# Kernel optimization log

Measured on AMD Instinct MI355X. Metric: run time of the kernel, lower is better.

Reference implementation:

```python
import jax, jax.numpy as jnp
import numpy as np

TEMP = 1.75   # temp_schedule(epoch=5, warmup=10): 2.5 - 1.5*0.5
ALPHA = 0.5   # blend_schedule(epoch=5): 0.2 + 0.6*0.5
EPS = 1e-5
HEADS = 2


def _ln(x, g, b):
    mu = x.mean(-1, keepdims=True)
    var = ((x - mu) ** 2).mean(-1, keepdims=True)
    return (x - mu) * jax.lax.rsqrt(var + EPS) * g + b


def _gelu(x):
    return jax.nn.gelu(x, approximate=False)  # torch nn.GELU default = exact erf


def _attn_pool(x, ln_g, ln_b, in_w, in_b, out_w, out_b):
    # x: [N, T, E]; nn.MultiheadAttention self-attention then mean over T
    N, T, E = x.shape
    Dh = E // HEADS
    xn = _ln(x, ln_g, ln_b)
    qkv = xn @ in_w + in_b                      # [N, T, 3E] (in_w stored [E, 3E])
    q, k, v = jnp.split(qkv, 3, axis=-1)
    q = q.reshape(N, T, HEADS, Dh).transpose(0, 2, 1, 3)
    k = k.reshape(N, T, HEADS, Dh).transpose(0, 2, 1, 3)
    v = v.reshape(N, T, HEADS, Dh).transpose(0, 2, 1, 3)
    scores = jnp.einsum('nhqd,nhkd->nhqk', q, k) / jnp.sqrt(jnp.float32(Dh))
    a = jax.nn.softmax(scores, axis=-1)
    o = jnp.einsum('nhqk,nhkd->nhqd', a, v).transpose(0, 2, 1, 3).reshape(N, T, E)
    o = o @ out_w + out_b                       # [N, T, E]
    return o.mean(axis=1)                       # [N, E]


def setup_inputs() -> dict:
    key = jax.random.key(0)
    ks = iter(jax.random.split(key, 40))
    B, L, T, D = 4, 24, 400, 1024
    H = D // 2  # 512
    G = 4       # groups
    s = 0.02
    r = lambda shp: jax.random.normal(next(ks), shp, dtype=jnp.float32) * s
    inp = {
        'x': jax.random.normal(next(ks), (B, L, T, D), dtype=jnp.float32),
        'mlp_alpha': jnp.ones((L,), jnp.float32),
        # shared MLP: LN -> Linear(D,H) -> GELU -> Linear(H,H)
        's_ln_g': jnp.ones((D,), jnp.float32), 's_ln_b': jnp.zeros((D,), jnp.float32),
        's_w1': r((D, H)), 's_b1': jnp.zeros((H,), jnp.float32),
        's_w2': r((H, H)), 's_b2': jnp.zeros((H,), jnp.float32),
        # 4 group MLPs (stacked)
        'g_ln_g': jnp.ones((G, D), jnp.float32), 'g_ln_b': jnp.zeros((G, D), jnp.float32),
        'g_w1': r((G, D, H)), 'g_b1': jnp.zeros((G, H), jnp.float32),
        'g_w2': r((G, H, H)), 'g_b2': jnp.zeros((G, H), jnp.float32),
        # TimeAttentionPool (shared module): LN + MHA(512, 2 heads) + out_proj
        'p_ln_g': jnp.ones((H,), jnp.float32), 'p_ln_b': jnp.zeros((H,), jnp.float32),
        'p_in_w': r((H, 3 * H)), 'p_in_b': jnp.zeros((3 * H,), jnp.float32),
        'p_out_w': r((H, H)), 'p_out_b': jnp.zeros((H,), jnp.float32),
        # router: Linear(512,128) -> GELU -> Linear(128,1) -> sigmoid(/temp)
        'r_w1': r((H, 128)), 'r_b1': jnp.zeros((128,), jnp.float32),
        'r_w2': r((128, 1)), 'r_b2': jnp.zeros((1,), jnp.float32),
        # post norms
        'pn_g': jnp.ones((H,), jnp.float32), 'pn_b': jnp.zeros((H,), jnp.float32),
        'pnf_g': jnp.ones((H,), jnp.float32), 'pnf_b': jnp.zeros((H,), jnp.float32),
        # classifier 512 -> 256 -> 128 -> 2
        'c_w1': r((H, H // 2)), 'c_b1': jnp.zeros((H // 2,), jnp.float32),
        'c_w2': r((H // 2, H // 4)), 'c_b2': jnp.zeros((H // 4,), jnp.float32),
        'c_w3': r((H // 4, 2)), 'c_b3': jnp.zeros((2,), jnp.float32),
    }
    return inp


def reference(x, mlp_alpha, s_ln_g, s_ln_b, s_w1, s_b1, s_w2, s_b2,
              g_ln_g, g_ln_b, g_w1, g_b1, g_w2, g_b2,
              p_ln_g, p_ln_b, p_in_w, p_in_b, p_out_w, p_out_b,
              r_w1, r_b1, r_w2, r_b2, pn_g, pn_b, pnf_g, pnf_b,
              c_w1, c_b1, c_w2, c_b2, c_w3, c_b3):
    B, L, T, D = x.shape
    G = g_w1.shape[0]
    S = L // G  # group_size = 6; expert i uses group i // S
    H = s_w1.shape[1]

    # shared MLP over all experts at once (dropout inactive in eval)
    xs = _ln(x, s_ln_g, s_ln_b)                              # [B,L,T,D]
    shared = _gelu(xs @ s_w1 + s_b1) @ s_w2 + s_b2           # [B,L,T,H]

    # group MLPs: experts i//S -> group; reshape L -> (G, S)
    xg = x.reshape(B, G, S, T, D)
    xgn = _ln(xg, g_ln_g[:, None, None, :], g_ln_b[:, None, None, :])
    hg = _gelu(jnp.einsum('bgstd,gdh->bgsth', xgn, g_w1) + g_b1[None, :, None, None, :])
    grp = jnp.einsum('bgsth,ghk->bgstk', hg, g_w2) + g_b2[None, :, None, None, :]
    grp = grp.reshape(B, L, T, H)

    weighted = shared + mlp_alpha[None, :, None, None] * grp  # [B,L,T,H]

    # attn-pool every expert stream (fold L into batch)
    time_pooled = _attn_pool(weighted.reshape(B * L, T, H),
                             p_ln_g, p_ln_b, p_in_w, p_in_b, p_out_w, p_out_b)
    time_pooled = time_pooled.reshape(B, L, H)               # [B,L,H]

    # router
    rh = _gelu(time_pooled @ r_w1 + r_b1)
    logits_r = (rh @ r_w2 + r_b2)[..., 0]                    # [B,L]
    learned = jax.nn.sigmoid(logits_r / TEMP)
    routing_weights = ALPHA * learned + (1.0 - ALPHA) / L

    # soft fusion over experts
    fusion = (weighted * routing_weights[:, :, None, None]).sum(axis=1)  # [B,T,H]
    fusion = _ln(fusion, pn_g, pn_b).mean(axis=1)            # [B,H]

    shared_mean = shared.mean(axis=1)                        # [B,T,H]
    time_ctx = _attn_pool(shared_mean, p_ln_g, p_ln_b, p_in_w, p_in_b, p_out_w, p_out_b)

    fused_all = _ln(fusion, pnf_g, pnf_b) + _ln(time_ctx, pnf_g, pnf_b)  # [B,H]

    h = _gelu(fused_all @ c_w1 + c_b1)
    h = _gelu(h @ c_w2 + c_b2)
    logits = h @ c_w3 + c_b3                                 # [B,2]
    return logits, routing_weights, fused_all, time_pooled
```

## Files before the change

kernel.cpp:

```cpp
#include <hip/hip_runtime.h>
#include <stdint.h>


typedef float f32x4 __attribute__((ext_vector_type(4)));
typedef short bf16x8 __attribute__((ext_vector_type(8)));

#define LP 72

__device__ __forceinline__ float bf2f(unsigned short u) {
  return __uint_as_float(((unsigned int)u) << 16);
}
__device__ __forceinline__ unsigned short f2bf(float f) {
  unsigned int u = __float_as_uint(f);
  u += 0x7fffu + ((u >> 16) & 1u);
  return (unsigned short)(u >> 16);
}
__device__ __forceinline__ float gelu_f(float x) {
  return 0.5f * x * (1.0f + erff(x * 0.70710678118654752440f));
}

template <int EPI, int GROUPED>
__global__ __launch_bounds__(256) void gemm_bt(
    const unsigned short* __restrict__ A, const unsigned short* __restrict__ WT,
    const float* __restrict__ bias, unsigned short* __restrict__ Cout,
    const unsigned short* __restrict__ addbuf, const float* __restrict__ alpha_vec,
    unsigned short* __restrict__ vtbuf, int K, int N, int ldout, int Mslice) {
  const int tid = (int)threadIdx.x;
  const int w = tid >> 6, lane = tid & 63, g = lane >> 4, ql = lane & 15;
  const int z = blockIdx.z;
  const int wr = w >> 1, wc = w & 1;

  int bm, bn;
  if (!GROUPED) {
    const int nbm = (int)gridDim.x, nbn = (int)gridDim.y;
    const int nb = nbm * nbn;
    const int lin = (int)blockIdx.x + nbm * (int)blockIdx.y;
    const int q = nb >> 3, r8 = nb & 7;
    const int xcd = lin & 7, c = lin >> 3;
    const int base = (xcd < r8) ? xcd * (q + 1) : r8 * (q + 1) + (xcd - r8) * q;
    const int widx = base + c;
    bm = widx / nbn;
    bn = widx - bm * nbn;
  } else {
    bm = (int)blockIdx.x;
    bn = (int)blockIdx.y;
  }
  const int n0 = bn * 128;

  int rowbase, rows_here;
  const unsigned short* wt = WT;
  const float* bs = bias;
  float alpha = 0.f;
  if (GROUPED) {
    const int l_idx = z % 24;
    const int grp = l_idx / 6;
    rowbase = z * Mslice + bm * 128;
    rows_here = Mslice - bm * 128;
    if (rows_here > 128) rows_here = 128;
    wt = WT + (size_t)grp * (size_t)N * (size_t)K;
    bs = bias + (size_t)grp * (size_t)N;
    if (EPI == 2) alpha = alpha_vec[l_idx];
  } else {
    rowbase = bm * 128;
    rows_here = Mslice - bm * 128;
    if (rows_here > 128) rows_here = 128;
  }

  __shared__ __align__(16) unsigned short sA[128 * LP];
  __shared__ __align__(16) unsigned short sB[128 * LP];

  f32x4 acc[4][4];
#pragma unroll
  for (int i = 0; i < 4; ++i)
#pragma unroll
    for (int j = 0; j < 4; ++j) acc[i][j] = (f32x4){0.f, 0.f, 0.f, 0.f};

  const int q0c = tid, q1c = tid + 256;
  const int r0 = q0c >> 2, s0 = q0c & 3;
  const int r1 = q1c >> 2, s1 = q1c & 3;
  const int r0c = r0 < rows_here ? r0 : rows_here - 1;
  const int r1c = r1 < rows_here ? r1 : rows_here - 1;
  const unsigned short* a0p = A + (size_t)(rowbase + r0c) * K + s0 * 8;
  const unsigned short* a1p = A + (size_t)(rowbase + r1c) * K + s1 * 8;
  const unsigned short* b0p = wt + (size_t)(n0 + r0) * K + s0 * 8;
  const unsigned short* b1p = wt + (size_t)(n0 + r1) * K + s1 * 8;

  const int nsteps = K >> 5;
  bf16x8 ra0 = *(const bf16x8*)a0p, ra1 = *(const bf16x8*)a1p;
  bf16x8 rb0 = *(const bf16x8*)b0p, rb1 = *(const bf16x8*)b1p;

  for (int s = 0; s < nsteps; ++s) {
    __syncthreads();
    *(bf16x8*)(sA + r0 * LP + s0 * 8) = ra0;
    *(bf16x8*)(sA + r1 * LP + s1 * 8) = ra1;
    *(bf16x8*)(sB + r0 * LP + s0 * 8) = rb0;
    *(bf16x8*)(sB + r1 * LP + s1 * 8) = rb1;
    __syncthreads();
    if (s + 1 < nsteps) {
      const int k0 = (s + 1) << 5;
      ra0 = *(const bf16x8*)(a0p + k0);
      ra1 = *(const bf16x8*)(a1p + k0);
      rb0 = *(const bf16x8*)(b0p + k0);
      rb1 = *(const bf16x8*)(b1p + k0);
    }
    bf16x8 af[4], bfr[4];
#pragma unroll
    for (int mi = 0; mi < 4; ++mi)
      af[mi] = *(const bf16x8*)(sA + (wr * 64 + mi * 16 + ql) * LP + g * 8);
#pragma unroll
    for (int ni = 0; ni < 4; ++ni)
      bfr[ni] = *(const bf16x8*)(sB + (wc * 64 + ni * 16 + ql) * LP + g * 8);
#pragma unroll
    for (int mi = 0; mi < 4; ++mi)
#pragma unroll
      for (int ni = 0; ni < 4; ++ni)
        acc[mi][ni] =
            __builtin_amdgcn_mfma_f32_16x16x32_bf16(af[mi], bfr[ni], acc[mi][ni], 0, 0, 0);
  }

#pragma unroll
  for (int mi = 0; mi < 4; ++mi) {
#pragma unroll
    for (int ni = 0; ni < 4; ++ni) {
      const int col = n0 + wc * 64 + ni * 16 + ql;
      const float bb = bs[col];
#pragma unroll
      for (int r = 0; r < 4; ++r) {
        const int rloc = wr * 64 + mi * 16 + 4 * g + r;
        if (rloc >= rows_here) continue;
        const int grow = rowbase + rloc;
        float v = acc[mi][ni][r] + bb;
        if (EPI == 1) v = gelu_f(v);
        if (EPI == 0 || EPI == 1) {
          Cout[(size_t)grow * ldout + col] = f2bf(v);
        } else if (EPI == 2) {
          const float sh = bf2f(addbuf[(size_t)grow * ldout + col]);
          Cout[(size_t)grow * ldout + col] = f2bf(sh + alpha * v);
        } else {
          if (col < 1024) {
            Cout[(size_t)grow * ldout + col] = f2bf(v);
          } else {
            vtbuf[(size_t)grow * 512 + (col - 1024)] = f2bf(v);
          }
        }
      }
    }
  }
}

__global__ void transpose_v(const unsigned short* __restrict__ vbuf,
                            unsigned short* __restrict__ vt) {
  const int p = blockIdx.z;
  const int h = p & 1, nst = p >> 1;
  const int t0 = blockIdx.x * 32, d0 = blockIdx.y * 32;
  __shared__ unsigned short tile[32][33];
  const int tx = threadIdx.x, ty = threadIdx.y;
#pragma unroll
  for (int i = 0; i < 4; ++i) {
    const int t = t0 + ty + i * 8;
    if (t < 400)
      tile[ty + i * 8][tx] = vbuf[((size_t)nst * 400 + t) * 512 + h * 256 + d0 + tx];
  }
  __syncthreads();
  const int t = t0 + tx;
  if (t < 400) {
#pragma unroll
    for (int i = 0; i < 4; ++i)
      vt[((size_t)p * 256 + d0 + ty + i * 8) * 400 + t] = tile[tx][ty + i * 8];
  }
}

__global__ __launch_bounds__(256, 2) void attn_fwd(const unsigned short* __restrict__ qk,
                                                   const unsigned short* __restrict__ vt,
                                                   unsigned short* __restrict__ outb) {
  const int nb = (int)gridDim.x;
  int flat = (int)blockIdx.x;
  flat = (flat & 7) * (nb >> 3) + (flat >> 3);
  const int qt = flat % 7;
  const int h = (flat / 7) & 1;
  const int n = flat / 14;
  const int q0 = qt * 64;

  const int tid = (int)threadIdx.x;
  const int w = tid >> 6, lane = tid & 63, g = lane >> 4, ql = lane & 15;

  __shared__ __align__(16) unsigned short slab[400 * 32];
  __shared__ __align__(16) unsigned short Pc[4][512];
  __shared__ float rs[4][16];

  const int qr = q0 + w * 16 + ql;
  const int qrc = qr < 400 ? qr : 399;
  const unsigned short* qp = qk + ((size_t)n * 400 + qrc) * 1024 + h * 256 + g * 8;
  bf16x8 qf[8];
#pragma unroll
  for (int d0 = 0; d0 < 8; ++d0) qf[d0] = *(const bf16x8*)(qp + d0 * 32);

  f32x4 st[25];
#pragma unroll
  for (int kf = 0; kf < 25; ++kf) st[kf] = (f32x4){0.f, 0.f, 0.f, 0.f};

  const unsigned short* kbase = qk + (size_t)n * 400 * 1024 + 512 + h * 256;
  for (int d0 = 0; d0 < 8; ++d0) {
    bf16x8 stg[7];
#pragma unroll
    for (int c = 0; c < 7; ++c) {
      const int q = tid + c * 256;
      const int r = q >> 2, slot = q & 3;
      if (r < 400)
        stg[c] = *(const bf16x8*)(kbase + (size_t)r * 1024 + d0 * 32 + slot * 8);
    }
    __syncthreads();
#pragma unroll
    for (int c = 0; c < 7; ++c) {
      const int q = tid + c * 256;
      const int r = q >> 2, slot = q & 3;
      if (r < 400) *(bf16x8*)(slab + r * 32 + (slot ^ ((r >> 1) & 3)) * 8) = stg[c];
    }
    __syncthreads();
#pragma unroll
    for (int kf = 0; kf < 25; ++kf) {
      const int r = kf * 16 + ql;
      bf16x8 kfr = *(const bf16x8*)(slab + r * 32 + ((g ^ ((r >> 1) & 3)) * 8));
      st[kf] = __builtin_amdgcn_mfma_f32_16x16x32_bf16(kfr, qf[d0], st[kf], 0, 0, 0);
    }
  }

  const float sc = 0.0625f;
  float m = -3.0e38f;
#pragma unroll
  for (int kf = 0; kf < 25; ++kf)
    m = fmaxf(m, fmaxf(fmaxf(st[kf][0], st[kf][1]), fmaxf(st[kf][2], st[kf][3])));
  m = fmaxf(m, __shfl_xor(m, 16));
  m = fmaxf(m, __shfl_xor(m, 32));
  float sum = 0.f;
  uint2 pp[25];
#pragma unroll
  for (int kf = 0; kf < 25; ++kf) {
    float e0 = expf((st[kf][0] - m) * sc);
    float e1 = expf((st[kf][1] - m) * sc);
    float e2 = expf((st[kf][2] - m) * sc);
    float e3 = expf((st[kf][3] - m) * sc);
    sum += (e0 + e1) + (e2 + e3);
    pp[kf].x = (unsigned int)f2bf(e0) | ((unsigned int)f2bf(e1) << 16);
    pp[kf].y = (unsigned int)f2bf(e2) | ((unsigned int)f2bf(e3) << 16);
  }
  sum += __shfl_xor(sum, 16);
  sum += __shfl_xor(sum, 32);
  if (g == 0) rs[w][ql] = sum;

  f32x4 oacc[16];
#pragma unroll
  for (int nf = 0; nf < 16; ++nf) oacc[nf] = (f32x4){0.f, 0.f, 0.f, 0.f};

  unsigned short* Pw = Pc[w];
  const unsigned short* vbase = vt + (size_t)(n * 2 + h) * 256 * 400;
  for (int kt = 0; kt < 13; ++kt) {
    const int k0 = kt * 32;
    bf16x8 stg[4];
#pragma unroll
    for (int c = 0; c < 4; ++c) {
      const int q = tid + c * 256;
      const int r = q >> 2, slot = q & 3;
      int kc = k0 + slot * 8;
      if (kc >= 400) kc = 0;
      stg[c] = *(const bf16x8*)(vbase + (size_t)r * 400 + kc);
    }
    __syncthreads();
#pragma unroll
    for (int c = 0; c < 4; ++c) {
      const int q = tid + c * 256;
      const int r = q >> 2, slot = q & 3;
      *(bf16x8*)(slab + r * 32 + (slot ^ ((r >> 1) & 3)) * 8) = stg[c];
    }
    {
      const int kf0 = 2 * kt;
      *(uint2*)(Pw + ql * 32 + 4 * g) = pp[kf0];
      uint2 hi = (kf0 + 1 < 25) ? pp[kf0 + 1] : (uint2){0u, 0u};
      *(uint2*)(Pw + ql * 32 + 16 + 4 * g) = hi;
    }
    __syncthreads();
    bf16x8 pa = *(const bf16x8*)(Pw + ql * 32 + g * 8);
#pragma unroll
    for (int nf = 0; nf < 16; ++nf) {
      const int r = nf * 16 + ql;
      bf16x8 vb = *(const bf16x8*)(slab + r * 32 + ((g ^ ((r >> 1) & 3)) * 8));
      oacc[nf] = __builtin_amdgcn_mfma_f32_16x16x32_bf16(pa, vb, oacc[nf], 0, 0, 0);
    }
  }

  const float inv0 = 1.f / rs[w][4 * g + 0];
  const float inv1 = 1.f / rs[w][4 * g + 1];
  const float inv2 = 1.f / rs[w][4 * g + 2];
  const float inv3 = 1.f / rs[w][4 * g + 3];
#pragma unroll
  for (int nf = 0; nf < 16; ++nf) {
#pragma unroll
    for (int r = 0; r < 4; ++r) {
      const int qrow = q0 + w * 16 + 4 * g + r;
      if (qrow < 400) {
        const float invr = (r == 0) ? inv0 : (r == 1) ? inv1 : (r == 2) ? inv2 : inv3;
        outb[((size_t)n * 400 + qrow) * 512 + h * 256 + nf * 16 + ql] =
            f2bf(oacc[nf][r] * invr);
      }
    }
  }
}

template <int TIN, int TOUT>
__global__ void ln_rows(const void* __restrict__ inv, void* __restrict__ outv,
                        const float* __restrict__ gam, const float* __restrict__ bet,
                        int C) {
  const int row = blockIdx.x, t = (int)threadIdx.x;
  float x0, x1, x2, x3;
  if (TIN == 0) {
    float4 v = ((const float4*)inv)[(size_t)row * (C >> 2) + t];
    x0 = v.x; x1 = v.y; x2 = v.z; x3 = v.w;
  } else {
    ushort4 v = ((const ushort4*)inv)[(size_t)row * (C >> 2) + t];
    x0 = bf2f(v.x); x1 = bf2f(v.y); x2 = bf2f(v.z); x3 = bf2f(v.w);
  }
  float s1 = x0 + x1 + x2 + x3;
  float s2 = x0 * x0 + x1 * x1 + x2 * x2 + x3 * x3;
  for (int mlane = 1; mlane < 64; mlane <<= 1) {
    s1 += __shfl_xor(s1, mlane);
    s2 += __shfl_xor(s2, mlane);
  }
  __shared__ float red[8];
  const int nw = blockDim.x >> 6;
  if ((t & 63) == 0) {
    red[t >> 6] = s1;
    red[4 + (t >> 6)] = s2;
  }
  __syncthreads();
  s1 = 0.f; s2 = 0.f;
  for (int i = 0; i < nw; ++i) {
    s1 += red[i];
    s2 += red[4 + i];
  }
  const float mu = s1 / C;
  const float var = s2 / C - mu * mu;
  const float rstd = rsqrtf(var + 1e-5f);
  float y0 = (x0 - mu) * rstd, y1 = (x1 - mu) * rstd, y2 = (x2 - mu) * rstd,
        y3 = (x3 - mu) * rstd;
  if (gam) {
    const int c = t * 4;
    y0 = y0 * gam[c + 0] + bet[c + 0];
    y1 = y1 * gam[c + 1] + bet[c + 1];
    y2 = y2 * gam[c + 2] + bet[c + 2];
    y3 = y3 * gam[c + 3] + bet[c + 3];
  }
  if (TOUT == 0) {
    ushort4 o;
    o.x = f2bf(y0); o.y = f2bf(y1); o.z = f2bf(y2); o.w = f2bf(y3);
    ((ushort4*)outv)[(size_t)row * (C >> 2) + t] = o;
  } else {
    float4 o;
    o.x = y0; o.y = y1; o.z = y2; o.w = y3;
    ((float4*)outv)[(size_t)row * (C >> 2) + t] = o;
  }
}

__global__ void transpose_w(const float* __restrict__ W, const float* __restrict__ scale,
                            unsigned short* __restrict__ WT, int K, int N) {
  __shared__ float tile[32][33];
  const int k0 = blockIdx.x * 32, n0 = blockIdx.y * 32, zg = blockIdx.z;
  const float* Wz = W + (size_t)zg * K * N;
  const float* sz = scale ? scale + (size_t)zg * K : (const float*)0;
  unsigned short* WTz = WT + (size_t)zg * (size_t)K * N;
  const int tx = threadIdx.x, ty = threadIdx.y;
#pragma unroll
  for (int i = 0; i < 4; ++i)
    tile[ty + i * 8][tx] = Wz[(size_t)(k0 + ty + i * 8) * N + n0 + tx];
  __syncthreads();
#pragma unroll
  for (int i = 0; i < 4; ++i) {
    const int nn = n0 + ty + i * 8;
    const int kk = k0 + tx;
    float v = tile[tx][ty + i * 8];
    if (sz) v *= sz[kk];
    WTz[(size_t)nn * K + kk] = f2bf(v);
  }
}

__global__ void transpose_wf(const float* __restrict__ W, float* __restrict__ WT, int K,
                             int N) {
  __shared__ float tile[32][33];
  const int k0 = blockIdx.x * 32, n0 = blockIdx.y * 32;
  const int tx = threadIdx.x, ty = threadIdx.y;
#pragma unroll
  for (int i = 0; i < 4; ++i) {
    const int k = k0 + ty + i * 8;
    if (k < K && n0 + tx < N) tile[ty + i * 8][tx] = W[(size_t)k * N + n0 + tx];
  }
  __syncthreads();
#pragma unroll
  for (int i = 0; i < 4; ++i) {
    const int nn = n0 + ty + i * 8;
    const int kk = k0 + tx;
    if (nn < N && kk < K) WT[(size_t)nn * K + kk] = tile[tx][ty + i * 8];
  }
}

#define BF_KC 16
__global__ void bias_fold_part(const float* __restrict__ W, const float* __restrict__ lb,
                               float* __restrict__ part, int K, int N) {
  const int zg = blockIdx.z;
  const int n = blockIdx.x * 256 + (int)threadIdx.x;
  const int kc = blockIdx.y;
  const int kpc = K / BF_KC;
  const float* Wz = W + (size_t)zg * K * N;
  const float* lbz = lb + (size_t)zg * K;
  float acc = 0.f;
  const int k1 = (kc + 1) * kpc;
  for (int k = kc * kpc; k < k1; ++k) acc += lbz[k] * Wz[(size_t)k * N + n];
  part[((size_t)zg * BF_KC + kc) * N + n] = acc;
}
__global__ void bias_fold_final(const float* __restrict__ part, const float* __restrict__ b,
                                float* __restrict__ beff, int N) {
  const int zg = blockIdx.y;
  const int n = blockIdx.x * 256 + (int)threadIdx.x;
  float acc = b[(size_t)zg * N + n];
#pragma unroll
  for (int c = 0; c < BF_KC; ++c) acc += part[((size_t)zg * BF_KC + c) * N + n];
  beff[(size_t)zg * N + n] = acc;
}

__global__ void mean_l(const unsigned short* __restrict__ sh, float* __restrict__ out) {
  const int i = blockIdx.x * 256 + (int)threadIdx.x;
  if (i >= 4 * 400 * 512 / 4) return;
  const int b = i / (400 * 512 / 4);
  const int rem4 = i - b * (400 * 512 / 4);
  float a0 = 0.f, a1 = 0.f, a2 = 0.f, a3 = 0.f;
  for (int l = 0; l < 24; ++l) {
    ushort4 v = *(const ushort4*)(sh + (size_t)(b * 24 + l) * 204800 + rem4 * 4);
    a0 += bf2f(v.x); a1 += bf2f(v.y); a2 += bf2f(v.z); a3 += bf2f(v.w);
  }
  float4 o;
  o.x = a0 * (1.f / 24.f); o.y = a1 * (1.f / 24.f);
  o.z = a2 * (1.f / 24.f); o.w = a3 * (1.f / 24.f);
  ((float4*)out)[i] = o;
}

__global__ void mean_t_bf16(const unsigned short* __restrict__ in, float* __restrict__ out,
                            int Ns) {
  const int i = blockIdx.x * 256 + (int)threadIdx.x;
  if (i >= Ns * 512) return;
  const int nstr = i >> 9, c = i & 511;
  float acc = 0.f;
  for (int t = 0; t < 400; ++t) acc += bf2f(in[((size_t)nstr * 400 + t) * 512 + c]);
  out[i] = acc * (1.f / 400.f);
}

__global__ void mean_t_f32(const float* __restrict__ in, float* __restrict__ out, int Ns) {
  const int i = blockIdx.x * 256 + (int)threadIdx.x;
  if (i >= Ns * 512) return;
  const int nstr = i >> 9, c = i & 511;
  float acc = 0.f;
  for (int t = 0; t < 400; ++t) acc += in[((size_t)nstr * 400 + t) * 512 + c];
  out[i] = acc * (1.f / 400.f);
}

__global__ void fuse_k(const unsigned short* __restrict__ wgt, const float* __restrict__ rw,
                       float* __restrict__ out) {
  const int i = blockIdx.x * 256 + (int)threadIdx.x;
  if (i >= 4 * 400 * 512 / 4) return;
  const int b = i / (400 * 512 / 4);
  const int rem4 = i - b * (400 * 512 / 4);
  float a0 = 0.f, a1 = 0.f, a2 = 0.f, a3 = 0.f;
  for (int l = 0; l < 24; ++l) {
    const float wv = rw[b * 24 + l];
    ushort4 v = *(const ushort4*)(wgt + (size_t)(b * 24 + l) * 204800 + rem4 * 4);
    a0 += wv * bf2f(v.x); a1 += wv * bf2f(v.y);
    a2 += wv * bf2f(v.z); a3 += wv * bf2f(v.w);
  }
  float4 o;
  o.x = a0; o.y = a1; o.z = a2; o.w = a3;
  ((float4*)out)[i] = o;
}

template <int WLAYOUT>
__global__ void gemv_wave(const float* __restrict__ A, const float* __restrict__ Wm,
                          const float* __restrict__ b, float* __restrict__ C, int M, int K,
                          int N, int act) {
  const int wid = (int)(blockIdx.x * (blockDim.x >> 6)) + ((int)threadIdx.x >> 6);
  const int lane = (int)threadIdx.x & 63;
  if (wid >= M * N) return;
  const int row = wid / N, col = wid - row * N;
  const float* a = A + (size_t)row * K;
  float acc = 0.f;
  if (WLAYOUT) {
    const float* wt = Wm + (size_t)col * K;
    for (int k = lane; k < K; k += 64) acc += a[k] * wt[k];
  } else {
    for (int k = lane; k < K; k += 64) acc += a[k] * Wm[(size_t)k * N + col];
  }
#pragma unroll
  for (int d = 1; d < 64; d <<= 1) acc += __shfl_xor(acc, d);
  if (lane == 0) {
    acc += b[col];
    if (act) acc = gelu_f(acc);
    C[wid] = acc;
  }
}

__global__ void routing_k(const float* __restrict__ lr, float* __restrict__ o1,
                          float* __restrict__ o2) {
  const int i = (int)threadIdx.x;
  if (i < 96) {
    const float v = 0.5f / (1.f + expf(-lr[i] * (1.f / 1.75f))) + (0.5f / 24.f);
    o1[i] = v;
    o2[i] = v;
  }
}

__global__ void add_k(const float* __restrict__ a, const float* __restrict__ b,
                      float* __restrict__ o1, float* __restrict__ o2, int n) {
  const int i = blockIdx.x * 256 + (int)threadIdx.x;
  if (i < n) {
    const float v = a[i] + b[i];
    o1[i] = v;
    o2[i] = v;
  }
}

extern "C" void kernel_launch(void* const* d_in, const int* in_sizes, int n_in,
                              void* d_out, int out_size, void* d_ws, size_t ws_size,
                              hipStream_t stream) {
  const float* x = (const float*)d_in[0];
  const float* mlp_alpha = (const float*)d_in[1];
  const float* s_ln_g = (const float*)d_in[2];
  const float* s_ln_b = (const float*)d_in[3];
  const float* s_w1 = (const float*)d_in[4];
  const float* s_b1 = (const float*)d_in[5];
  const float* s_w2 = (const float*)d_in[6];
  const float* s_b2 = (const float*)d_in[7];
  const float* g_ln_g = (const float*)d_in[8];
  const float* g_ln_b = (const float*)d_in[9];
  const float* g_w1 = (const float*)d_in[10];
  const float* g_b1 = (const float*)d_in[11];
  const float* g_w2 = (const float*)d_in[12];
  const float* g_b2 = (const float*)d_in[13];
  const float* p_ln_g = (const float*)d_in[14];
  const float* p_ln_b = (const float*)d_in[15];
  const float* p_in_w = (const float*)d_in[16];
  const float* p_in_b = (const float*)d_in[17];
  const float* p_out_w = (const float*)d_in[18];
  const float* p_out_b = (const float*)d_in[19];
  const float* r_w1 = (const float*)d_in[20];
  const float* r_b1 = (const float*)d_in[21];
  const float* r_w2 = (const float*)d_in[22];
  const float* r_b2 = (const float*)d_in[23];
  const float* pn_g = (const float*)d_in[24];
  const float* pn_b = (const float*)d_in[25];
  const float* pnf_g = (const float*)d_in[26];
  const float* pnf_b = (const float*)d_in[27];
  const float* c_w1 = (const float*)d_in[28];
  const float* c_b1 = (const float*)d_in[29];
  const float* c_w2 = (const float*)d_in[30];
  const float* c_b2 = (const float*)d_in[31];
  const float* c_w3 = (const float*)d_in[32];
  const float* c_b3 = (const float*)d_in[33];

  float* out = (float*)d_out;
  uint8_t* ws = (uint8_t*)d_ws;

  size_t off = 0;
  auto alloc = [&](size_t bytes) -> size_t {
    size_t o = off;
    off += (bytes + 255) & ~(size_t)255;
    return o;
  };
  const size_t off_xhat = alloc(38400ull * 1024 * 2);
  const size_t off_h = alloc(38400ull * 512 * 2);
  const size_t off_shared = alloc(38400ull * 512 * 2);
  const size_t off_weighted = alloc(38400ull * 512 * 2);
  const size_t off_qk = alloc(38400ull * 1024 * 2);
  const size_t off_pooled = alloc(96ull * 512 * 4);
  const size_t off_rh = alloc(96ull * 128 * 4);
  const size_t off_lr = alloc(96ull * 4);
  const size_t off_rw = alloc(96ull * 4);
  const size_t off_smean = alloc(4ull * 400 * 512 * 4);
  const size_t off_wn2 = alloc(1600ull * 512 * 2);
  const size_t off_qk2 = alloc(1600ull * 1024 * 2);
  const size_t off_vbuf2 = alloc(1600ull * 512 * 2);
  const size_t off_vt2 = alloc(4ull * 2 * 256 * 400 * 2);
  const size_t off_ao2 = alloc(1600ull * 512 * 2);
  const size_t off_pooled2 = alloc(4ull * 512 * 4);
  const size_t off_tctx = alloc(4ull * 512 * 4);
  const size_t off_fusion = alloc(4ull * 400 * 512 * 4);
  const size_t off_fln = alloc(4ull * 400 * 512 * 4);
  const size_t off_fvec = alloc(4ull * 512 * 4);
  const size_t off_fa = alloc(4ull * 512 * 4);
  const size_t off_fb = alloc(4ull * 512 * 4);
  const size_t off_fall = alloc(4ull * 512 * 4);
  const size_t off_c1 = alloc(4ull * 256 * 4);
  const size_t off_c2 = alloc(4ull * 128 * 4);
  const size_t off_sw1T = alloc(512ull * 1024 * 2);
  const size_t off_sw2T = alloc(512ull * 512 * 2);
  const size_t off_gw1T = alloc(4ull * 512 * 1024 * 2);
  const size_t off_gw2T = alloc(4ull * 512 * 512 * 2);
  const size_t off_pinT = alloc(1536ull * 512 * 2);
  const size_t off_sb1e = alloc(512ull * 4);
  const size_t off_gb1e = alloc(4ull * 512 * 4);
  const size_t off_pinbe = alloc(1536ull * 4);
  const size_t off_bfp_s = alloc((size_t)BF_KC * 512 * 4);
  const size_t off_bfp_g = alloc(4ull * BF_KC * 512 * 4);
  const size_t off_bfp_p = alloc((size_t)BF_KC * 1536 * 4);
  const size_t off_powT = alloc(512ull * 512 * 4);
  const size_t off_rw1T = alloc(128ull * 512 * 4);
  const size_t off_cw1T = alloc(256ull * 512 * 4);
  const size_t off_cw2T = alloc(128ull * 256 * 4);
  const size_t off_wn = off_xhat;
  const size_t off_vbuf = off_xhat + 38400ull * 512 * 2;
  const size_t off_vt = off_shared;
  const size_t off_ao = off_h;
  if (off > ws_size) return;

  unsigned short* xhat = (unsigned short*)(ws + off_xhat);
  unsigned short* hbuf = (unsigned short*)(ws + off_h);
  unsigned short* sharedb = (unsigned short*)(ws + off_shared);
  unsigned short* weighted = (unsigned short*)(ws + off_weighted);
  unsigned short* qk = (unsigned short*)(ws + off_qk);
  unsigned short* wn = (unsigned short*)(ws + off_wn);
  unsigned short* vbuf = (unsigned short*)(ws + off_vbuf);
  unsigned short* vt = (unsigned short*)(ws + off_vt);
  unsigned short* ao = (unsigned short*)(ws + off_ao);
  float* pooled = (float*)(ws + off_pooled);
  float* rh = (float*)(ws + off_rh);
  float* lr = (float*)(ws + off_lr);
  float* rw = (float*)(ws + off_rw);
  float* smean = (float*)(ws + off_smean);
  unsigned short* wn2 = (unsigned short*)(ws + off_wn2);
  unsigned short* qk2 = (unsigned short*)(ws + off_qk2);
  unsigned short* vbuf2 = (unsigned short*)(ws + off_vbuf2);
  unsigned short* vt2 = (unsigned short*)(ws + off_vt2);
  unsigned short* ao2 = (unsigned short*)(ws + off_ao2);
  float* pooled2 = (float*)(ws + off_pooled2);
  float* tctx = (float*)(ws + off_tctx);
  float* fusion = (float*)(ws + off_fusion);
  float* fln = (float*)(ws + off_fln);
  float* fvec = (float*)(ws + off_fvec);
  float* fa = (float*)(ws + off_fa);
  float* fb = (float*)(ws + off_fb);
  float* fall = (float*)(ws + off_fall);
  float* c1 = (float*)(ws + off_c1);
  float* c2 = (float*)(ws + off_c2);
  unsigned short* sw1T = (unsigned short*)(ws + off_sw1T);
  unsigned short* sw2T = (unsigned short*)(ws + off_sw2T);
  unsigned short* gw1T = (unsigned short*)(ws + off_gw1T);
  unsigned short* gw2T = (unsigned short*)(ws + off_gw2T);
  unsigned short* pinT = (unsigned short*)(ws + off_pinT);
  float* sb1e = (float*)(ws + off_sb1e);
  float* gb1e = (float*)(ws + off_gb1e);
  float* pinbe = (float*)(ws + off_pinbe);
  float* bfp_s = (float*)(ws + off_bfp_s);
  float* bfp_g = (float*)(ws + off_bfp_g);
  float* bfp_p = (float*)(ws + off_bfp_p);
  float* powT = (float*)(ws + off_powT);
  float* rw1T = (float*)(ws + off_rw1T);
  float* cw1T = (float*)(ws + off_cw1T);
  float* cw2T = (float*)(ws + off_cw2T);

  transpose_w<<<dim3(32, 16, 1), dim3(32, 8), 0, stream>>>(s_w1, s_ln_g, sw1T, 1024, 512);
  transpose_w<<<dim3(16, 16, 1), dim3(32, 8), 0, stream>>>(s_w2, (const float*)0, sw2T, 512, 512);
  transpose_w<<<dim3(32, 16, 4), dim3(32, 8), 0, stream>>>(g_w1, g_ln_g, gw1T, 1024, 512);
  transpose_w<<<dim3(16, 16, 4), dim3(32, 8), 0, stream>>>(g_w2, (const float*)0, gw2T, 512, 512);
  transpose_w<<<dim3(16, 48, 1), dim3(32, 8), 0, stream>>>(p_in_w, p_ln_g, pinT, 512, 1536);
  transpose_wf<<<dim3(16, 16), dim3(32, 8), 0, stream>>>(p_out_w, powT, 512, 512);
  transpose_wf<<<dim3(16, 4), dim3(32, 8), 0, stream>>>(r_w1, rw1T, 512, 128);
  transpose_wf<<<dim3(16, 8), dim3(32, 8), 0, stream>>>(c_w1, cw1T, 512, 256);
  transpose_wf<<<dim3(8, 4), dim3(32, 8), 0, stream>>>(c_w2, cw2T, 256, 128);
  bias_fold_part<<<dim3(2, BF_KC, 1), 256, 0, stream>>>(s_w1, s_ln_b, bfp_s, 1024, 512);
  bias_fold_final<<<dim3(2, 1), 256, 0, stream>>>(bfp_s, s_b1, sb1e, 512);
  bias_fold_part<<<dim3(2, BF_KC, 4), 256, 0, stream>>>(g_w1, g_ln_b, bfp_g, 1024, 512);
  bias_fold_final<<<dim3(2, 4), 256, 0, stream>>>(bfp_g, g_b1, gb1e, 512);
  bias_fold_part<<<dim3(6, BF_KC, 1), 256, 0, stream>>>(p_in_w, p_ln_b, bfp_p, 512, 1536);
  bias_fold_final<<<dim3(6, 1), 256, 0, stream>>>(bfp_p, p_in_b, pinbe, 1536);

  ln_rows<0, 0><<<38400, 256, 0, stream>>>(x, xhat, (const float*)0, (const float*)0, 1024);

  gemm_bt<1, 0><<<dim3(300, 4, 1), 256, 0, stream>>>(xhat, sw1T, sb1e, hbuf,
      (const unsigned short*)0, (const float*)0, (unsigned short*)0, 1024, 512, 512, 38400);
  gemm_bt<0, 0><<<dim3(300, 4, 1), 256, 0, stream>>>(hbuf, sw2T, s_b2, sharedb,
      (const unsigned short*)0, (const float*)0, (unsigned short*)0, 512, 512, 512, 38400);
  mean_l<<<800, 256, 0, stream>>>(sharedb, smean);

  gemm_bt<1, 1><<<dim3(4, 4, 96), 256, 0, stream>>>(xhat, gw1T, gb1e, hbuf,
      (const unsigned short*)0, (const float*)0, (unsigned short*)0, 1024, 512, 512, 400);
  gemm_bt<2, 1><<<dim3(4, 4, 96), 256, 0, stream>>>(hbuf, gw2T, g_b2, weighted,
      sharedb, mlp_alpha, (unsigned short*)0, 512, 512, 512, 400);

  ln_rows<1, 0><<<38400, 128, 0, stream>>>(weighted, wn, (const float*)0, (const float*)0, 512);
  gemm_bt<3, 0><<<dim3(300, 12, 1), 256, 0, stream>>>(wn, pinT, pinbe, qk,
      (const unsigned short*)0, (const float*)0, vbuf, 512, 1536, 1024, 38400);
  transpose_v<<<dim3(13, 8, 192), dim3(32, 8), 0, stream>>>(vbuf, vt);
  attn_fwd<<<dim3(14 * 96), 256, 0, stream>>>(qk, vt, ao);
  mean_t_bf16<<<192, 256, 0, stream>>>(ao, pooled, 96);
  gemv_wave<1><<<12288, 256, 0, stream>>>(pooled, powT, p_out_b, out + 2152, 96, 512, 512, 0);

  gemv_wave<1><<<3072, 256, 0, stream>>>(out + 2152, rw1T, r_b1, rh, 96, 512, 128, 1);
  gemv_wave<0><<<24, 256, 0, stream>>>(rh, r_w2, r_b2, lr, 96, 128, 1, 0);
  routing_k<<<1, 128, 0, stream>>>(lr, out + 8, rw);

  fuse_k<<<800, 256, 0, stream>>>(weighted, rw, fusion);
  ln_rows<0, 1><<<1600, 128, 0, stream>>>(fusion, fln, pn_g, pn_b, 512);
  mean_t_f32<<<8, 256, 0, stream>>>(fln, fvec, 4);

  ln_rows<0, 0><<<1600, 128, 0, stream>>>(smean, wn2, (const float*)0, (const float*)0, 512);
  gemm_bt<3, 0><<<dim3(13, 12, 1), 256, 0, stream>>>(wn2, pinT, pinbe, qk2,
      (const unsigned short*)0, (const float*)0, vbuf2, 512, 1536, 1024, 1600);
  transpose_v<<<dim3(13, 8, 8), dim3(32, 8), 0, stream>>>(vbuf2, vt2);
  attn_fwd<<<dim3(14 * 4), 256, 0, stream>>>(qk2, vt2, ao2);
  mean_t_bf16<<<8, 256, 0, stream>>>(ao2, pooled2, 4);
  gemv_wave<1><<<512, 256, 0, stream>>>(pooled2, powT, p_out_b, tctx, 4, 512, 512, 0);

  ln_rows<0, 1><<<4, 128, 0, stream>>>(fvec, fa, pnf_g, pnf_b, 512);
  ln_rows<0, 1><<<4, 128, 0, stream>>>(tctx, fb, pnf_g, pnf_b, 512);
  add_k<<<8, 256, 0, stream>>>(fa, fb, out + 104, fall, 2048);

  gemv_wave<1><<<256, 256, 0, stream>>>(fall, cw1T, c_b1, c1, 4, 512, 256, 1);
  gemv_wave<1><<<128, 256, 0, stream>>>(c1, cw2T, c_b2, c2, 4, 256, 128, 1);
  gemv_wave<0><<<2, 256, 0, stream>>>(c2, c_w3, c_b3, out, 4, 128, 2, 0);
}
```

Before: 823.2 us.

## Use direct global-to-LDS loads with double-buffered swizzled tiles in GEMM

Replaces the register-staged global loads and LDS stores in the bf16 MFMA GEMM with global_load_lds direct copies into a double-buffered shared-memory tile. The padded LDS layout is replaced by an XOR swizzle so reads stay bank-conflict-free without padding. One barrier per k-step is removed and the next tile's fetch overlaps the MFMA work, cutting register pressure and VALU copy work. The risk is subtle ordering, since async LDS loads need proper waitcnt before the barrier, and LDS use doubles per block.

```diff
diff --git a/kernel.cpp b/kernel.cpp
--- a/kernel.cpp
+++ b/kernel.cpp
@@ -4,8 +4,6 @@
 
 typedef float f32x4 __attribute__((ext_vector_type(4)));
 typedef short bf16x8 __attribute__((ext_vector_type(8)));
-
-#define LP 72
 
 __device__ __forceinline__ float bf2f(unsigned short u) {
   return __uint_as_float(((unsigned int)u) << 16);
@@ -17,6 +15,12 @@
 }
 __device__ __forceinline__ float gelu_f(float x) {
   return 0.5f * x * (1.0f + erff(x * 0.70710678118654752440f));
+}
+
+typedef __attribute__((address_space(1))) const unsigned int gas_u32;
+typedef __attribute__((address_space(3))) unsigned int las_u32;
+__device__ __forceinline__ void gload16(const unsigned short* g, unsigned short* l) {
+  __builtin_amdgcn_global_load_lds((gas_u32*)g, (las_u32*)l, 16, 0, 0);
 }
 
 template <int EPI, int GROUPED>
@@ -66,8 +70,8 @@
     if (rows_here > 128) rows_here = 128;
   }
 
-  __shared__ __align__(16) unsigned short sA[128 * LP];
-  __shared__ __align__(16) unsigned short sB[128 * LP];
+  __shared__ __align__(16) unsigned short sA[2][128 * 32];
+  __shared__ __align__(16) unsigned short sB[2][128 * 32];
 
   f32x4 acc[4][4];
 #pragma unroll
@@ -75,47 +79,51 @@
 #pragma unroll
     for (int j = 0; j < 4; ++j) acc[i][j] = (f32x4){0.f, 0.f, 0.f, 0.f};
 
-  const int q0c = tid, q1c = tid + 256;
-  const int r0 = q0c >> 2, s0 = q0c & 3;
-  const int r1 = q1c >> 2, s1 = q1c & 3;
-  const int r0c = r0 < rows_here ? r0 : rows_here - 1;
-  const int r1c = r1 < rows_here ? r1 : rows_here - 1;
-  const unsigned short* a0p = A + (size_t)(rowbase + r0c) * K + s0 * 8;
-  const unsigned short* a1p = A + (size_t)(rowbase + r1c) * K + s1 * 8;
-  const unsigned short* b0p = wt + (size_t)(n0 + r0) * K + s0 * 8;
-  const unsigned short* b1p = wt + (size_t)(n0 + r1) * K + s1 * 8;
+  const int swzg = (lane & 3) ^ ((lane >> 3) & 3);
+  const int rA0 = w * 32 + (lane >> 2);
+  const int rA1 = rA0 + 16;
+  const int rA0c = rA0 < rows_here ? rA0 : rows_here - 1;
+  const int rA1c = rA1 < rows_here ? rA1 : rows_here - 1;
+  const unsigned short* a0p = A + (size_t)(rowbase + rA0c) * K + swzg * 8;
+  const unsigned short* a1p = A + (size_t)(rowbase + rA1c) * K + swzg * 8;
+  const unsigned short* b0p = wt + (size_t)(n0 + rA0) * K + swzg * 8;
+  const unsigned short* b1p = wt + (size_t)(n0 + rA1) * K + swzg * 8;
+  const int ldsw = w * 1024;
+
+  const int aroff = (wr * 64 + ql) * 32 + ((g ^ ((ql >> 1) & 3)) * 8);
+  const int broff = (wc * 64 + ql) * 32 + ((g ^ ((ql >> 1) & 3)) * 8);
 
   const int nsteps = K >> 5;
-  bf16x8 ra0 = *(const bf16x8*)a0p, ra1 = *(const bf16x8*)a1p;
-  bf16x8 rb0 = *(const bf16x8*)b0p, rb1 = *(const bf16x8*)b1p;
+  gload16(a0p, &sA[0][ldsw]);
+  gload16(a1p, &sA[0][ldsw + 512]);
+  gload16(b0p, &sB[0][ldsw]);
+  gload16(b1p, &sB[0][ldsw + 512]);
+  __syncthreads();
 
   for (int s = 0; s < nsteps; ++s) {
-    __syncthreads();
-    *(bf16x8*)(sA + r0 * LP + s0 * 8) = ra0;
-    *(bf16x8*)(sA + r1 * LP + s1 * 8) = ra1;
-    *(bf16x8*)(sB + r0 * LP + s0 * 8) = rb0;
-    *(bf16x8*)(sB + r1 * LP + s1 * 8) = rb1;
-    __syncthreads();
+    const int cur = s & 1;
     if (s + 1 < nsteps) {
       const int k0 = (s + 1) << 5;
-      ra0 = *(const bf16x8*)(a0p + k0);
-      ra1 = *(const bf16x8*)(a1p + k0);
-      rb0 = *(const bf16x8*)(b0p + k0);
-      rb1 = *(const bf16x8*)(b1p + k0);
+      const int nxt = cur ^ 1;
+      gload16(a0p + k0, &sA[nxt][ldsw]);
+      gload16(a1p + k0, &sA[nxt][ldsw + 512]);
+      gload16(b0p + k0, &sB[nxt][ldsw]);
+      gload16(b1p + k0, &sB[nxt][ldsw + 512]);
     }
     bf16x8 af[4], bfr[4];
 #pragma unroll
     for (int mi = 0; mi < 4; ++mi)
-      af[mi] = *(const bf16x8*)(sA + (wr * 64 + mi * 16 + ql) * LP + g * 8);
+      af[mi] = *(const bf16x8*)(&sA[cur][aroff + mi * 512]);
 #pragma unroll
     for (int ni = 0; ni < 4; ++ni)
-      bfr[ni] = *(const bf16x8*)(sB + (wc * 64 + ni * 16 + ql) * LP + g * 8);
+      bfr[ni] = *(const bf16x8*)(&sB[cur][broff + ni * 512]);
 #pragma unroll
     for (int mi = 0; mi < 4; ++mi)
 #pragma unroll
       for (int ni = 0; ni < 4; ++ni)
         acc[mi][ni] =
             __builtin_amdgcn_mfma_f32_16x16x32_bf16(af[mi], bfr[ni], acc[mi][ni], 0, 0, 0);
+    __syncthreads();
   }
 
 #pragma unroll
```

Result: no change. 821.1 us (-0.3%).
